# Kernel optimization log

Measured on AMD Instinct MI355X. Metric: run time of the kernel, lower is better.

Reference implementation:

```python
import jax, jax.numpy as jnp
import numpy as np

B, N, H = 4, 1024, 32


def setup_inputs() -> dict:
    key = jax.random.key(0)
    ks = jax.random.split(key, 8)
    weights = jax.random.uniform(ks[0], (B, N), dtype=jnp.float32)
    distances = jax.random.uniform(ks[1], (B, N, N), dtype=jnp.float32)
    # nn.Linear-style params (kaiming-uniform-ish scale: U(-1/sqrt(fan_in), 1/sqrt(fan_in)))
    def lin(k, fan_in, fan_out):
        k1, k2 = jax.random.split(k)
        bound = 1.0 / np.sqrt(fan_in)
        W = jax.random.uniform(k1, (fan_in, fan_out), minval=-bound, maxval=bound, dtype=jnp.float32)
        b = jax.random.uniform(k2, (fan_out,), minval=-bound, maxval=bound, dtype=jnp.float32)
        return W, b
    W1, b1 = lin(ks[2], 3, H)
    W2, b2 = lin(ks[3], H, H)
    W3, b3 = lin(ks[4], H, 1)
    return {"weights": weights, "distances": distances,
            "W1": W1, "b1": b1, "W2": W2, "b2": b2, "W3": W3, "b3": b3}


def reference(weights, distances, W1, b1, W2, b2, W3, b3):
    # Avoid materializing the stacked [B,N,N,3] tensor: since the first layer
    # is linear, split W1 rows and broadcast-add the three contributions.
    # h1[b,i,j,:] = w_i * W1[0] + w_j * W1[1] + d_ij * W1[2] + b1
    wi = weights[:, :, None, None] * W1[0]            # [B,N,1,H]
    wj = weights[:, None, :, None] * W1[1]            # [B,1,N,H]
    h = wi + wj + distances[..., None] * W1[2] + b1   # [B,N,N,H]
    h = jax.nn.relu(h)
    h = jax.nn.relu(jnp.einsum('bijh,hk->bijk', h, W2) + b2)
    out = jnp.einsum('bijh,ho->bijo', h, W3) + b3     # [B,N,N,1]
    return jax.nn.softplus(out[..., 0])               # [B,N,N]
```

## Files before the change

kernel.cpp:

```cpp
#include <hip/hip_runtime.h>

#define HCH 32
#define NDIM 1024
#define SEG 512
#define PAIRS (SEG / 64)

using half2v   = __attribute__((ext_vector_type(2))) _Float16;
using half8    = __attribute__((ext_vector_type(8))) _Float16;
using floatx16 = __attribute__((ext_vector_type(16))) float;

__global__ __launch_bounds__(256, 4)
void lf_kernel(const float* __restrict__ weights,
               const float* __restrict__ distances,
               const float* __restrict__ W1,
               const float* __restrict__ b1,
               const float* __restrict__ W2,
               const float* __restrict__ b2,
               const float* __restrict__ W3,
               const float* __restrict__ b3,
               float* __restrict__ out)
{
    __shared__ float sd[4][SEG];
    __shared__ float sw[4][SEG];

    const int lane = threadIdx.x & 63;
    const int wv = threadIdx.x >> 6;
    const int wave_gid = __builtin_amdgcn_readfirstlane(blockIdx.x * 4 + wv);
    const int row_id = wave_gid >> 1;
    const int j_begin = (wave_gid & 1) * SEG;
    const int b = row_id >> 10;

    const int col = lane & 31;
    const int half_id = lane >> 5;
    const bool hi = (half_id != 0);
    const int kb = half_id * 8;

    const float* __restrict__ drow = distances + (size_t)row_id * NDIM + j_begin;
    const float* __restrict__ wrow = weights + b * NDIM + j_begin;
    float* __restrict__ orow = out + (size_t)row_id * NDIM + j_begin;

    const float4 dv0 = *(const float4*)(drow + 4 * lane);
    const float4 dv1 = *(const float4*)(drow + 256 + 4 * lane);
    const float4 wv0 = *(const float4*)(wrow + 4 * lane);
    const float4 wv1 = *(const float4*)(wrow + 256 + 4 * lane);

    const float wi = weights[row_id];

    half2v base2[8], cc2[8], ee2[8];
#pragma unroll
    for (int p = 0; p < 8; ++p) {
        const int chA = (p < 4) ? (kb + 2 * p) : (16 + kb + 2 * (p - 4));
        const int chB = chA + 1;
        base2[p] = half2v{(_Float16)fmaf(W1[chA], wi, b1[chA]),
                          (_Float16)fmaf(W1[chB], wi, b1[chB])};
        cc2[p] = half2v{(_Float16)W1[HCH + chA], (_Float16)W1[HCH + chB]};
        ee2[p] = half2v{(_Float16)W1[2 * HCH + chA], (_Float16)W1[2 * HCH + chB]};
    }

    half8 a0, a1;
#pragma unroll
    for (int j = 0; j < 8; ++j) {
        a0[j] = (_Float16)W2[(kb + j) * HCH + col];
        a1[j] = (_Float16)W2[(16 + kb + j) * HCH + col];
    }

    floatx16 cinit;
    float w3r[16];
#pragma unroll
    for (int r = 0; r < 16; ++r) {
        const int rc = (r & 3) + 8 * (r >> 2) + 4 * half_id;
        cinit[r] = b2[rc];
        w3r[r]   = W3[rc];
    }
    const float b3v = b3[0];

    *(float4*)&sd[wv][4 * lane]       = dv0;
    *(float4*)&sd[wv][256 + 4 * lane] = dv1;
    *(float4*)&sw[wv][4 * lane]       = wv0;
    *(float4*)&sw[wv][256 + 4 * lane] = wv1;
    __syncthreads();

    const half2v zero2 = half2v{(_Float16)0.0f, (_Float16)0.0f};

#pragma unroll
    for (int p = 0; p < PAIRS; ++p) {
        const float dA = sd[wv][p * 64 + col];
        const float dB = sd[wv][p * 64 + 32 + col];
        const float wA = sw[wv][p * 64 + col];
        const float wB = sw[wv][p * 64 + 32 + col];

        const _Float16 dhA = (_Float16)dA, wjhA = (_Float16)wA;
        const _Float16 dhB = (_Float16)dB, wjhB = (_Float16)wB;
        const half2v d2A = half2v{dhA, dhA}, wj2A = half2v{wjhA, wjhA};
        const half2v d2B = half2v{dhB, dhB}, wj2B = half2v{wjhB, wjhB};

        union Frag { half8 v; half2v h[4]; } f0A, f1A, f0B, f1B;
#pragma unroll
        for (int q = 0; q < 4; ++q) {
            half2v tA0 = __builtin_elementwise_fma(cc2[q], wj2A, base2[q]);
            tA0 = __builtin_elementwise_fma(ee2[q], d2A, tA0);
            f0A.h[q] = __builtin_elementwise_max(tA0, zero2);
            half2v tA1 = __builtin_elementwise_fma(cc2[q + 4], wj2A, base2[q + 4]);
            tA1 = __builtin_elementwise_fma(ee2[q + 4], d2A, tA1);
            f1A.h[q] = __builtin_elementwise_max(tA1, zero2);
            half2v tB0 = __builtin_elementwise_fma(cc2[q], wj2B, base2[q]);
            tB0 = __builtin_elementwise_fma(ee2[q], d2B, tB0);
            f0B.h[q] = __builtin_elementwise_max(tB0, zero2);
            half2v tB1 = __builtin_elementwise_fma(cc2[q + 4], wj2B, base2[q + 4]);
            tB1 = __builtin_elementwise_fma(ee2[q + 4], d2B, tB1);
            f1B.h[q] = __builtin_elementwise_max(tB1, zero2);
        }

        floatx16 accA = __builtin_amdgcn_mfma_f32_32x32x16_f16(a0, f0A.v, cinit, 0, 0, 0);
        floatx16 accB = __builtin_amdgcn_mfma_f32_32x32x16_f16(a0, f0B.v, cinit, 0, 0, 0);
        accA = __builtin_amdgcn_mfma_f32_32x32x16_f16(a1, f1A.v, accA, 0, 0, 0);
        accB = __builtin_amdgcn_mfma_f32_32x32x16_f16(a1, f1B.v, accB, 0, 0, 0);

        float sA0 = 0.0f, sA1 = 0.0f, sB0 = 0.0f, sB1 = 0.0f;
#pragma unroll
        for (int r = 0; r < 16; r += 2) {
            sA0 = fmaf(fmaxf(accA[r + 0], 0.0f), w3r[r + 0], sA0);
            sA1 = fmaf(fmaxf(accA[r + 1], 0.0f), w3r[r + 1], sA1);
            sB0 = fmaf(fmaxf(accB[r + 0], 0.0f), w3r[r + 0], sB0);
            sB1 = fmaf(fmaxf(accB[r + 1], 0.0f), w3r[r + 1], sB1);
        }
        const float sA = sA0 + sA1;
        const float sB = sB0 + sB1;

        const float u = hi ? sA : sB;
        const float other = __shfl_xor(u, 32, 64);
        const float loc = hi ? sB : sA;
        const float full = loc + other;

        const float x = full + b3v;
        const float sp = fmaxf(x, 0.0f) + __logf(1.0f + __expf(-fabsf(x)));

        orow[p * 64 + lane] = sp;

    }
}

extern "C" void kernel_launch(void* const* d_in, const int* in_sizes, int n_in,
                              void* d_out, int out_size, void* d_ws, size_t ws_size,
                              hipStream_t stream) {
    const float* weights   = (const float*)d_in[0];
    const float* distances = (const float*)d_in[1];
    const float* W1 = (const float*)d_in[2];
    const float* b1 = (const float*)d_in[3];
    const float* W2 = (const float*)d_in[4];
    const float* b2 = (const float*)d_in[5];
    const float* W3 = (const float*)d_in[6];
    const float* b3 = (const float*)d_in[7];
    float* out = (float*)d_out;

    const int rows_total = 4 * 1024;
    dim3 grid(rows_total * (NDIM / SEG) / 4);
    lf_kernel<<<grid, 256, 0, stream>>>(weights, distances, W1, b1, W2, b2, W3, b3, out);
}
```

Baseline: 101.4 us.

## Process multiple half-rows per wave with double-buffered LDS prefetch

Makes each wave loop over four half-row units instead of one, shrinking the grid to a fixed 512 blocks and amortizing per-wave setup of weight fragments. The next unit's distance and weight vectors are loaded into registers during compute and stored into an alternate LDS buffer, overlapping global loads with math. The block barrier is removed since each wave only touches its own LDS slice. This trades away occupancy and parallel slack, and the row bias term is now computed in fp16.

```diff
diff --git a/kernel.cpp b/kernel.cpp
--- a/kernel.cpp
+++ b/kernel.cpp
@@ -4,6 +4,8 @@
 #define NDIM 1024
 #define SEG 512
 #define PAIRS (SEG / 64)
+#define HRPW 4
+#define NBLOCKS 512
 
 using half2v   = __attribute__((ext_vector_type(2))) _Float16;
 using half8    = __attribute__((ext_vector_type(8))) _Float16;
@@ -20,41 +22,37 @@
                const float* __restrict__ b3,
                float* __restrict__ out)
 {
-    __shared__ float sd[4][SEG];
-    __shared__ float sw[4][SEG];
+    __shared__ float sd[4][2][SEG];
+    __shared__ float sw[4][2][SEG];
 
     const int lane = threadIdx.x & 63;
     const int wv = threadIdx.x >> 6;
-    const int wave_gid = __builtin_amdgcn_readfirstlane(blockIdx.x * 4 + wv);
-    const int row_id = wave_gid >> 1;
-    const int j_begin = (wave_gid & 1) * SEG;
-    const int b = row_id >> 10;
+    const int wave_gid = blockIdx.x * 4 + wv;
+    const int unit0 = wave_gid * HRPW;
 
     const int col = lane & 31;
     const int half_id = lane >> 5;
     const bool hi = (half_id != 0);
     const int kb = half_id * 8;
 
-    const float* __restrict__ drow = distances + (size_t)row_id * NDIM + j_begin;
-    const float* __restrict__ wrow = weights + b * NDIM + j_begin;
-    float* __restrict__ orow = out + (size_t)row_id * NDIM + j_begin;
+    const int r0 = unit0 >> 1;
+    const int jb0 = (unit0 & 1) * SEG;
+    const float* __restrict__ dr0 = distances + (size_t)r0 * NDIM + jb0;
+    const float* __restrict__ wr0 = weights + (r0 >> 10) * NDIM + jb0;
+    const float4 d0 = *(const float4*)(dr0 + 4 * lane);
+    const float4 d1 = *(const float4*)(dr0 + 256 + 4 * lane);
+    const float4 w0 = *(const float4*)(wr0 + 4 * lane);
+    const float4 w1v = *(const float4*)(wr0 + 256 + 4 * lane);
 
-    const float4 dv0 = *(const float4*)(drow + 4 * lane);
-    const float4 dv1 = *(const float4*)(drow + 256 + 4 * lane);
-    const float4 wv0 = *(const float4*)(wrow + 4 * lane);
-    const float4 wv1 = *(const float4*)(wrow + 256 + 4 * lane);
-
-    const float wi = weights[row_id];
-
-    half2v base2[8], cc2[8], ee2[8];
+    half2v cc2[8], ee2[8], w10h[8], b10h[8];
 #pragma unroll
     for (int p = 0; p < 8; ++p) {
         const int chA = (p < 4) ? (kb + 2 * p) : (16 + kb + 2 * (p - 4));
         const int chB = chA + 1;
-        base2[p] = half2v{(_Float16)fmaf(W1[chA], wi, b1[chA]),
-                          (_Float16)fmaf(W1[chB], wi, b1[chB])};
-        cc2[p] = half2v{(_Float16)W1[HCH + chA], (_Float16)W1[HCH + chB]};
-        ee2[p] = half2v{(_Float16)W1[2 * HCH + chA], (_Float16)W1[2 * HCH + chB]};
+        cc2[p]  = half2v{(_Float16)W1[HCH + chA],     (_Float16)W1[HCH + chB]};
+        ee2[p]  = half2v{(_Float16)W1[2 * HCH + chA], (_Float16)W1[2 * HCH + chB]};
+        w10h[p] = half2v{(_Float16)W1[chA],           (_Float16)W1[chB]};
+        b10h[p] = half2v{(_Float16)b1[chA],           (_Float16)b1[chB]};
     }
 
     half8 a0, a1;
@@ -74,69 +72,99 @@
     }
     const float b3v = b3[0];
 
-    *(float4*)&sd[wv][4 * lane]       = dv0;
-    *(float4*)&sd[wv][256 + 4 * lane] = dv1;
-    *(float4*)&sw[wv][4 * lane]       = wv0;
-    *(float4*)&sw[wv][256 + 4 * lane] = wv1;
-    __syncthreads();
+    *(float4*)&sd[wv][0][4 * lane]       = d0;
+    *(float4*)&sd[wv][0][256 + 4 * lane] = d1;
+    *(float4*)&sw[wv][0][4 * lane]       = w0;
+    *(float4*)&sw[wv][0][256 + 4 * lane] = w1v;
 
     const half2v zero2 = half2v{(_Float16)0.0f, (_Float16)0.0f};
 
+    for (int t = 0; t < HRPW; ++t) {
+        const int unit = unit0 + t;
+        const int row_id = unit >> 1;
+        const int jb = (unit & 1) * SEG;
+        const int buf = t & 1;
+
+        const int un = (t + 1 < HRPW) ? (unit + 1) : unit0;
+        const int rn = un >> 1;
+        const int jbn = (un & 1) * SEG;
+        const float* __restrict__ drn = distances + (size_t)rn * NDIM + jbn;
+        const float* __restrict__ wrn = weights + (rn >> 10) * NDIM + jbn;
+        const float4 pd0 = *(const float4*)(drn + 4 * lane);
+        const float4 pd1 = *(const float4*)(drn + 256 + 4 * lane);
+        const float4 pw0 = *(const float4*)(wrn + 4 * lane);
+        const float4 pw1 = *(const float4*)(wrn + 256 + 4 * lane);
+
+        const float wi = weights[row_id];
+        const _Float16 wih = (_Float16)wi;
+        const half2v wi2 = half2v{wih, wih};
+        half2v base2[8];
 #pragma unroll
-    for (int p = 0; p < PAIRS; ++p) {
-        const float dA = sd[wv][p * 64 + col];
-        const float dB = sd[wv][p * 64 + 32 + col];
-        const float wA = sw[wv][p * 64 + col];
-        const float wB = sw[wv][p * 64 + 32 + col];
+        for (int p = 0; p < 8; ++p)
+            base2[p] = __builtin_elementwise_fma(w10h[p], wi2, b10h[p]);
 
-        const _Float16 dhA = (_Float16)dA, wjhA = (_Float16)wA;
-        const _Float16 dhB = (_Float16)dB, wjhB = (_Float16)wB;
-        const half2v d2A = half2v{dhA, dhA}, wj2A = half2v{wjhA, wjhA};
-        const half2v d2B = half2v{dhB, dhB}, wj2B = half2v{wjhB, wjhB};
+        float* __restrict__ orow = out + (size_t)row_id * NDIM + jb;
 
-        union Frag { half8 v; half2v h[4]; } f0A, f1A, f0B, f1B;
 #pragma unroll
-        for (int q = 0; q < 4; ++q) {
-            half2v tA0 = __builtin_elementwise_fma(cc2[q], wj2A, base2[q]);
-            tA0 = __builtin_elementwise_fma(ee2[q], d2A, tA0);
-            f0A.h[q] = __builtin_elementwise_max(tA0, zero2);
-            half2v tA1 = __builtin_elementwise_fma(cc2[q + 4], wj2A, base2[q + 4]);
-            tA1 = __builtin_elementwise_fma(ee2[q + 4], d2A, tA1);
-            f1A.h[q] = __builtin_elementwise_max(tA1, zero2);
-            half2v tB0 = __builtin_elementwise_fma(cc2[q], wj2B, base2[q]);
-            tB0 = __builtin_elementwise_fma(ee2[q], d2B, tB0);
-            f0B.h[q] = __builtin_elementwise_max(tB0, zero2);
-            half2v tB1 = __builtin_elementwise_fma(cc2[q + 4], wj2B, base2[q + 4]);
-            tB1 = __builtin_elementwise_fma(ee2[q + 4], d2B, tB1);
-            f1B.h[q] = __builtin_elementwise_max(tB1, zero2);
+        for (int p = 0; p < PAIRS; ++p) {
+            const float dA = sd[wv][buf][p * 64 + col];
+            const float dB = sd[wv][buf][p * 64 + 32 + col];
+            const float wA = sw[wv][buf][p * 64 + col];
+            const float wB = sw[wv][buf][p * 64 + 32 + col];
+
+            const _Float16 dhA = (_Float16)dA, wjhA = (_Float16)wA;
+            const _Float16 dhB = (_Float16)dB, wjhB = (_Float16)wB;
+            const half2v d2A = half2v{dhA, dhA}, wj2A = half2v{wjhA, wjhA};
+            const half2v d2B = half2v{dhB, dhB}, wj2B = half2v{wjhB, wjhB};
+
+            union Frag { half8 v; half2v h[4]; } f0A, f1A, f0B, f1B;
+#pragma unroll
+            for (int q = 0; q < 4; ++q) {
+                half2v tA0 = __builtin_elementwise_fma(cc2[q], wj2A, base2[q]);
+                tA0 = __builtin_elementwise_fma(ee2[q], d2A, tA0);
+                f0A.h[q] = __builtin_elementwise_max(tA0, zero2);
+                half2v tA1 = __builtin_elementwise_fma(cc2[q + 4], wj2A, base2[q + 4]);
+                tA1 = __builtin_elementwise_fma(ee2[q + 4], d2A, tA1);
+                f1A.h[q] = __builtin_elementwise_max(tA1, zero2);
+                half2v tB0 = __builtin_elementwise_fma(cc2[q], wj2B, base2[q]);
+                tB0 = __builtin_elementwise_fma(ee2[q], d2B, tB0);
+                f0B.h[q] = __builtin_elementwise_max(tB0, zero2);
+                half2v tB1 = __builtin_elementwise_fma(cc2[q + 4], wj2B, base2[q + 4]);
+                tB1 = __builtin_elementwise_fma(ee2[q + 4], d2B, tB1);
+                f1B.h[q] = __builtin_elementwise_max(tB1, zero2);
+            }
+
+            floatx16 accA = __builtin_amdgcn_mfma_f32_32x32x16_f16(a0, f0A.v, cinit, 0, 0, 0);
+            floatx16 accB = __builtin_amdgcn_mfma_f32_32x32x16_f16(a0, f0B.v, cinit, 0, 0, 0);
+            accA = __builtin_amdgcn_mfma_f32_32x32x16_f16(a1, f1A.v, accA, 0, 0, 0);
+            accB = __builtin_amdgcn_mfma_f32_32x32x16_f16(a1, f1B.v, accB, 0, 0, 0);
+
+            float sA0 = 0.0f, sA1 = 0.0f, sB0 = 0.0f, sB1 = 0.0f;
+#pragma unroll
+            for (int r = 0; r < 16; r += 2) {
+                sA0 = fmaf(fmaxf(accA[r + 0], 0.0f), w3r[r + 0], sA0);
+                sA1 = fmaf(fmaxf(accA[r + 1], 0.0f), w3r[r + 1], sA1);
+                sB0 = fmaf(fmaxf(accB[r + 0], 0.0f), w3r[r + 0], sB0);
+                sB1 = fmaf(fmaxf(accB[r + 1], 0.0f), w3r[r + 1], sB1);
+            }
+            const float sA = sA0 + sA1;
+            const float sB = sB0 + sB1;
+
+            const float u = hi ? sA : sB;
+            const float other = __shfl_xor(u, 32, 64);
+            const float loc = hi ? sB : sA;
+            const float full = loc + other;
+
+            const float x = full + b3v;
+            const float sp = fmaxf(x, 0.0f) + __logf(1.0f + __expf(-fabsf(x)));
+
+            orow[p * 64 + lane] = sp;
         }
 
-        floatx16 accA = __builtin_amdgcn_mfma_f32_32x32x16_f16(a0, f0A.v, cinit, 0, 0, 0);
-        floatx16 accB = __builtin_amdgcn_mfma_f32_32x32x16_f16(a0, f0B.v, cinit, 0, 0, 0);
-        accA = __builtin_amdgcn_mfma_f32_32x32x16_f16(a1, f1A.v, accA, 0, 0, 0);
-        accB = __builtin_amdgcn_mfma_f32_32x32x16_f16(a1, f1B.v, accB, 0, 0, 0);
-
-        float sA0 = 0.0f, sA1 = 0.0f, sB0 = 0.0f, sB1 = 0.0f;
-#pragma unroll
-        for (int r = 0; r < 16; r += 2) {
-            sA0 = fmaf(fmaxf(accA[r + 0], 0.0f), w3r[r + 0], sA0);
-            sA1 = fmaf(fmaxf(accA[r + 1], 0.0f), w3r[r + 1], sA1);
-            sB0 = fmaf(fmaxf(accB[r + 0], 0.0f), w3r[r + 0], sB0);
-            sB1 = fmaf(fmaxf(accB[r + 1], 0.0f), w3r[r + 1], sB1);
-        }
-        const float sA = sA0 + sA1;
-        const float sB = sB0 + sB1;
-
-        const float u = hi ? sA : sB;
-        const float other = __shfl_xor(u, 32, 64);
-        const float loc = hi ? sB : sA;
-        const float full = loc + other;
-
-        const float x = full + b3v;
-        const float sp = fmaxf(x, 0.0f) + __logf(1.0f + __expf(-fabsf(x)));
-
-        orow[p * 64 + lane] = sp;
-
+        *(float4*)&sd[wv][buf ^ 1][4 * lane]       = pd0;
+        *(float4*)&sd[wv][buf ^ 1][256 + 4 * lane] = pd1;
+        *(float4*)&sw[wv][buf ^ 1][4 * lane]       = pw0;
+        *(float4*)&sw[wv][buf ^ 1][256 + 4 * lane] = pw1;
     }
 }
 
@@ -153,7 +181,6 @@
     const float* b3 = (const float*)d_in[7];
     float* out = (float*)d_out;
 
-    const int rows_total = 4 * 1024;
-    dim3 grid(rows_total * (NDIM / SEG) / 4);
-    lf_kernel<<<grid, 256, 0, stream>>>(weights, distances, W1, b1, W2, b2, W3, b3, out);
+    lf_kernel<<<dim3(NBLOCKS), 256, 0, stream>>>(weights, distances,
+                                                 W1, b1, W2, b2, W3, b3, out);
 }
```

New measurement: 116.8 us. 1.15x slower.
